# Kernel tuning notes

Measured on AMD Instinct MI355X. Metric: run time of the kernel, lower is better.

The kernel has to match this reference:

```python
import jax, jax.numpy as jnp
import numpy as np

N_HEADS, DK, DV, G = 12, 64, 64, 1
W_WIN, R_RAND = 3, 2
B, S, D = 2, 2048, 768


def _make_idx_tensor(seq_len, g, w, r, seed=0):
    # Mirrors SparseMultiHeadAttention.create_idx_tensor: each middle row is
    # [0] + r random key indices + w consecutive window key indices.
    rng = np.random.default_rng(seed)
    s2 = seq_len - 2 * g
    shift = max(g - (w - 1) // 2, 0)
    windows = np.arange(s2)[:, None] + np.arange(w)[None, :] + shift  # (s2, w)
    rand = np.empty((s2, r), np.int64)
    half = (w - 1) // 2
    for i in range(s2):
        pos = i + g
        cand = rng.choice(np.arange(1, seq_len), size=r + w + 2, replace=False)
        cand = cand[np.abs(cand - pos) > half][:r]
        rand[i] = cand
    idx = np.concatenate([np.zeros((s2, 1), np.int64), rand, windows], axis=1)
    return jnp.asarray(idx)  # (s2, 1+r+w)


def setup_inputs() -> dict:
    key = jax.random.key(0)
    ks = jax.random.split(key, 7)
    scale = 0.02  # keep projected logits in a sane range for softmax
    return {
        "Q": jax.random.normal(ks[0], (B, S, D), jnp.float32),
        "K": jax.random.normal(ks[1], (B, S, D), jnp.float32),
        "V": jax.random.normal(ks[2], (B, S, D), jnp.float32),
        "Wq": jax.random.normal(ks[3], (N_HEADS * DK, D), jnp.float32) * scale,
        "Wk": jax.random.normal(ks[4], (N_HEADS * DK, D), jnp.float32) * scale,
        "Wv": jax.random.normal(ks[5], (N_HEADS * DV, D), jnp.float32) * scale,
        "Wo": jax.random.normal(ks[6], (D, N_HEADS * DV), jnp.float32) * scale,
        "idx_tensor": _make_idx_tensor(S, G, W_WIN, R_RAND),
    }


def reference(Q, K, V, Wq, Wk, Wv, Wo, idx_tensor):
    b, s, d = Q.shape
    h, dk, dv, g = N_HEADS, DK, DV, G
    # projections (torch Linear: x @ W.T), split heads -> (b, h, s, d_head)
    q = (Q @ Wq.T).reshape(b, s, h, dk).transpose(0, 2, 1, 3)
    k = (K @ Wk.T).reshape(b, s, h, dk).transpose(0, 2, 1, 3)
    v = (V @ Wv.T).reshape(b, s, h, dv).transpose(0, 2, 1, 3)

    # global rows (first g, last g) attend densely over all keys
    gidx = jnp.concatenate([jnp.arange(g), jnp.arange(s - g, s)])
    global_attn = jnp.einsum('bhgd,bhtd->bhgt', q[:, :, gidx, :], k)  # (b,h,2g,s)

    # middle rows: gather [first, random..., window...] keys per row
    comb = k[:, :, idx_tensor, :]                    # (b, h, s2, 1+r+w, dk)
    scores = jnp.einsum('bhsd,bhskd->bhsk', q[:, :, g:s - g, :], comb)

    # scatter into a dense (s, s) score matrix (zeros elsewhere), as the source does
    result = jnp.zeros((b, h, s, s), q.dtype)
    result = result.at[:, :, gidx, :].set(global_attn)
    rows = jnp.arange(g, s - g)[:, None]             # (s2, 1)
    result = result.at[:, :, rows, idx_tensor].set(scores)
    result = result / jnp.sqrt(jnp.asarray(dk, q.dtype))

    attn = jax.nn.softmax(result, axis=-1)
    out = jnp.einsum('bhst,bhtd->bhsd', attn, v)     # (b, h, s, dv)
    out = out.transpose(0, 2, 1, 3).reshape(b, s, h * dv)
    return out @ Wo.T
```

## Files before the change

### kernel.cpp

```cpp
#include <hip/hip_runtime.h>
#include <hip/hip_bf16.h>

#define S_LEN   2048
#define D_MODEL 768
#define NH      12
#define HD      64
#define NI      6
#define S2      2046
#define BB      2
#define NCH     8
#define CHK     256

typedef unsigned short ushort_t;
typedef __attribute__((ext_vector_type(8))) short short8v;
typedef __attribute__((ext_vector_type(4))) float f32x4;

__device__ __forceinline__ unsigned short bf16_rne(float x) {
    union { float f; unsigned int u; } c; c.f = x;
    unsigned int u = c.u + 0x7fffu + ((c.u >> 16) & 1u);
    return (unsigned short)(u >> 16);
}
__device__ __forceinline__ float bf16_f(unsigned short h) {
    union { unsigned int u; float f; } c; c.u = ((unsigned int)h) << 16;
    return c.f;
}

__device__ __forceinline__ void gload16(const ushort_t* g, ushort_t* l) {
    __builtin_amdgcn_global_load_lds(
        (const __attribute__((address_space(1))) void*)g,
        (__attribute__((address_space(3))) void*)l, 16, 0, 0);
}

struct Cvt4 {
    const float* s0; const float* s1; const float* s2; const float* s3;
    ushort_t* d0; ushort_t* d1; ushort_t* d2; ushort_t* d3;
};

__global__ __launch_bounds__(256) void cvt_kernel(Cvt4 a, int n) {
    const float* s; ushort_t* d;
    switch (blockIdx.z) {
        case 0: s = a.s0; d = a.d0; break;
        case 1: s = a.s1; d = a.d1; break;
        case 2: s = a.s2; d = a.d2; break;
        default: s = a.s3; d = a.d3; break;
    }
    const int i = (blockIdx.x * 256 + threadIdx.x) * 8;
    float4 v0 = *(const float4*)&s[i];
    float4 v1 = *(const float4*)&s[i + 4];
    short8v o;
    o[0] = (short)bf16_rne(v0.x); o[1] = (short)bf16_rne(v0.y);
    o[2] = (short)bf16_rne(v0.z); o[3] = (short)bf16_rne(v0.w);
    o[4] = (short)bf16_rne(v1.x); o[5] = (short)bf16_rne(v1.y);
    o[6] = (short)bf16_rne(v1.z); o[7] = (short)bf16_rne(v1.w);
    *(short8v*)&d[i] = o;
}

struct GemmArgs { const ushort_t* A; const ushort_t* W; ushort_t* C; float* Cf; };

constexpr int GK = 768, GN = 768, GBK = 32, GNT = GK / GBK;

__global__ __launch_bounds__(256) void bf16_gemm_nt(GemmArgs g0, GemmArgs g1, GemmArgs g2) {
    GemmArgs g = (blockIdx.z == 0) ? g0 : ((blockIdx.z == 1) ? g1 : g2);

    __shared__ ushort_t As[3][4096];
    __shared__ ushort_t Bs[3][4096];

    const int tid  = threadIdx.x;
    const int lane = tid & 63;
    const int w    = tid >> 6;
    const int wm   = w & 1;
    const int wn   = w >> 1;
    const int bm   = blockIdx.y * 128;
    const int bn   = blockIdx.x * 128;
    const int fr   = lane & 15;
    const int blkr = lane >> 4;

    f32x4 acc[4][4];
    #pragma unroll
    for (int i = 0; i < 4; ++i)
        #pragma unroll
        for (int j = 0; j < 4; ++j)
            acc[i][j] = (f32x4){0.f, 0.f, 0.f, 0.f};

    const int row0 = tid >> 2;
    const int row1 = row0 + 64;
    const int blk0 = (tid & 3) ^ ((row0 >> 1) & 3);
    const int blk1 = (tid & 3) ^ ((row1 >> 1) & 3);
    const ushort_t* Ag0 = g.A + (size_t)(bm + row0) * GK + blk0 * 8;
    const ushort_t* Ag1 = g.A + (size_t)(bm + row1) * GK + blk1 * 8;
    const ushort_t* Bg0 = g.W + (size_t)(bn + row0) * GK + blk0 * 8;
    const ushort_t* Bg1 = g.W + (size_t)(bn + row1) * GK + blk1 * 8;
    const int l0 = w * 512;
    const int l1 = 2048 + w * 512;

    int aoff[4], boff[4];
    #pragma unroll
    for (int i = 0; i < 4; ++i) {
        const int ra = wm * 64 + i * 16 + fr;
        aoff[i] = (ra * 4 + (blkr ^ ((ra >> 1) & 3))) * 8;
        const int rb = wn * 64 + i * 16 + fr;
        boff[i] = (rb * 4 + (blkr ^ ((rb >> 1) & 3))) * 8;
    }

    gload16(Ag0, &As[0][l0]); gload16(Ag1, &As[0][l1]);
    gload16(Bg0, &Bs[0][l0]); gload16(Bg1, &Bs[0][l1]);
    gload16(Ag0 + GBK, &As[1][l0]); gload16(Ag1 + GBK, &As[1][l1]);
    gload16(Bg0 + GBK, &Bs[1][l0]); gload16(Bg1 + GBK, &Bs[1][l1]);

    for (int t = 0; t < GNT; ++t) {
        if (t < GNT - 1) asm volatile("s_waitcnt vmcnt(4)" ::: "memory");
        else             asm volatile("s_waitcnt vmcnt(0)" ::: "memory");
        __builtin_amdgcn_s_barrier();

        if (t + 2 < GNT) {
            const int ko = (t + 2) * GBK;
            const int nb = (t + 2) % 3;
            gload16(Ag0 + ko, &As[nb][l0]); gload16(Ag1 + ko, &As[nb][l1]);
            gload16(Bg0 + ko, &Bs[nb][l0]); gload16(Bg1 + ko, &Bs[nb][l1]);
        }

        const ushort_t* as = As[t % 3];
        const ushort_t* bs = Bs[t % 3];
        short8v a[4], b[4];
        #pragma unroll
        for (int i = 0; i < 4; ++i) a[i] = *(const short8v*)&as[aoff[i]];
        #pragma unroll
        for (int i = 0; i < 4; ++i) b[i] = *(const short8v*)&bs[boff[i]];
        #pragma unroll
        for (int i = 0; i < 4; ++i)
            #pragma unroll
            for (int j = 0; j < 4; ++j)
                acc[i][j] = __builtin_amdgcn_mfma_f32_16x16x32_bf16(a[i], b[j], acc[i][j], 0, 0, 0);
    }

    const int crow0 = bm + wm * 64 + ((lane >> 4) << 2);
    const int ccol0 = bn + wn * 64 + fr;
    if (g.Cf) {
        #pragma unroll
        for (int i = 0; i < 4; ++i)
            #pragma unroll
            for (int j = 0; j < 4; ++j)
                #pragma unroll
                for (int r = 0; r < 4; ++r)
                    g.Cf[(size_t)(crow0 + i * 16 + r) * GN + ccol0 + j * 16] = acc[i][j][r];
    } else {
        #pragma unroll
        for (int i = 0; i < 4; ++i)
            #pragma unroll
            for (int j = 0; j < 4; ++j)
                #pragma unroll
                for (int r = 0; r < 4; ++r)
                    g.C[(size_t)(crow0 + i * 16 + r) * GN + ccol0 + j * 16] = bf16_rne(acc[i][j][r]);
    }
}

__global__ __launch_bounds__(256) void vsum_kernel(const ushort_t* __restrict__ v,
                                                   float* __restrict__ vsum) {
    const int b = blockIdx.x;
    const int c = blockIdx.y * 256 + threadIdx.x;
    const int s0 = blockIdx.z * 64;
    float a = 0.f;
    for (int s = s0; s < s0 + 64; ++s)
        a += bf16_f(v[((size_t)(b * S_LEN + s)) * D_MODEL + c]);
    atomicAdd(&vsum[b * D_MODEL + c], a);
}

__global__ __launch_bounds__(768) void sparse_attn(
    const ushort_t* __restrict__ q, const ushort_t* __restrict__ k, const ushort_t* __restrict__ v,
    const float* __restrict__ vsum, const int* __restrict__ idx,
    ushort_t* __restrict__ ao) {
    const int i = blockIdx.x;
    const int b = blockIdx.y;
    const int pos = i + 1;
    const int c = threadIdx.x;

    int id[NI];
    #pragma unroll
    for (int j = 0; j < NI; ++j) id[j] = idx[i * NI + j];
    bool dup[NI];
    #pragma unroll
    for (int j = 0; j < NI; ++j) {
        bool d = false;
        #pragma unroll
        for (int j2 = 0; j2 < NI; ++j2)
            if (j2 < j) d = d || (id[j2] == id[j]);
        dup[j] = d;
    }

    const size_t rowbase = ((size_t)(b * S_LEN + pos)) * D_MODEL;
    const float qv = bf16_f(q[rowbase + c]);

    float kv[NI], vv[NI];
    #pragma unroll
    for (int j = 0; j < NI; ++j) {
        const size_t kb = ((size_t)(b * S_LEN + id[j])) * D_MODEL + c;
        kv[j] = bf16_f(k[kb]);
        vv[j] = bf16_f(v[kb]);
    }

    float p[NI];
    #pragma unroll
    for (int j = 0; j < NI; ++j) p[j] = qv * kv[j];

    #pragma unroll
    for (int off = 32; off; off >>= 1) {
        #pragma unroll
        for (int j = 0; j < NI; ++j) p[j] += __shfl_xor(p[j], off);
    }

    float acc = vsum[b * D_MODEL + c];
    float Z = 0.f;
    int u = 0;
    #pragma unroll
    for (int j = 0; j < NI; ++j) {
        if (dup[j]) continue;
        float e = expf(p[j] * 0.125f);
        Z += e;
        u += 1;
        acc += (e - 1.f) * vv[j];
    }
    Z += (float)(S_LEN - u);
    ao[rowbase + c] = bf16_rne(acc / Z);
}

__global__ __launch_bounds__(256) void global_attn_part(
    const ushort_t* __restrict__ q, const ushort_t* __restrict__ k, const ushort_t* __restrict__ v,
    float* __restrict__ part) {
    const int ch = blockIdx.x;
    const int rowsel = blockIdx.y;
    const int row = rowsel ? (S_LEN - 1) : 0;
    const int hb = blockIdx.z;
    const int h = hb % NH;
    const int b = hb / NH;
    const int tid = threadIdx.x;

    __shared__ float qs[HD];
    __shared__ float ps[CHK];
    __shared__ float red[8];
    __shared__ float pacc[256];

    if (tid < HD) qs[tid] = bf16_f(q[((size_t)(b * S_LEN + row)) * D_MODEL + h * HD + tid]);
    __syncthreads();

    const int t = ch * CHK + tid;
    const ushort_t* kp = &k[((size_t)(b * S_LEN + t)) * D_MODEL + h * HD];
    float s = 0.f;
    #pragma unroll
    for (int dd = 0; dd < 8; ++dd) {
        short8v kk = *(const short8v*)&kp[dd * 8];
        #pragma unroll
        for (int e = 0; e < 8; ++e)
            s += qs[dd * 8 + e] * bf16_f((unsigned short)kk[e]);
    }
    s *= 0.125f;

    float m = s;
    #pragma unroll
    for (int off = 32; off; off >>= 1) m = fmaxf(m, __shfl_xor(m, off));
    if ((tid & 63) == 0) red[tid >> 6] = m;
    __syncthreads();
    m = fmaxf(fmaxf(red[0], red[1]), fmaxf(red[2], red[3]));

    float e = expf(s - m);
    ps[tid] = e;
    float zp = e;
    #pragma unroll
    for (int off = 32; off; off >>= 1) zp += __shfl_xor(zp, off);
    if ((tid & 63) == 0) red[4 + (tid >> 6)] = zp;
    __syncthreads();
    const float E = red[4] + red[5] + red[6] + red[7];

    const int d0 = tid & 63;
    const int grp = tid >> 6;
    float acc = 0.f;
    for (int tt = grp; tt < CHK; tt += 4)
        acc += ps[tt] * bf16_f(v[((size_t)(b * S_LEN + ch * CHK + tt)) * D_MODEL + h * HD + d0]);
    pacc[tid] = acc;
    __syncthreads();
    if (tid < HD) {
        float o = pacc[tid] + pacc[64 + tid] + pacc[128 + tid] + pacc[192 + tid];
        float* pr = part + ((size_t)((hb * 2 + rowsel) * NCH + ch)) * (HD + 2);
        pr[2 + tid] = o;
        if (tid == 0) { pr[0] = m; pr[1] = E; }
    }
}

__global__ __launch_bounds__(64) void global_attn_fin(
    const float* __restrict__ part, ushort_t* __restrict__ ao) {
    const int rb = blockIdx.x;
    const int rowsel = rb & 1;
    const int hb = rb >> 1;
    const int h = hb % NH;
    const int b = hb / NH;
    const int row = rowsel ? (S_LEN - 1) : 0;
    const int d = threadIdx.x;

    const float* pr = part + (size_t)rb * NCH * (HD + 2);
    float M = -1e30f;
    #pragma unroll
    for (int c = 0; c < NCH; ++c) M = fmaxf(M, pr[c * (HD + 2)]);
    float Z = 0.f, acc = 0.f;
    #pragma unroll
    for (int c = 0; c < NCH; ++c) {
        float wgt = expf(pr[c * (HD + 2)] - M);
        Z   += pr[c * (HD + 2) + 1] * wgt;
        acc += pr[c * (HD + 2) + 2 + d] * wgt;
    }
    ao[((size_t)(b * S_LEN + row)) * D_MODEL + h * HD + d] = bf16_rne(acc / Z);
}

extern "C" void kernel_launch(void* const* d_in, const int* in_sizes, int n_in,
                              void* d_out, int out_size, void* d_ws, size_t ws_size,
                              hipStream_t stream) {
    const float* Q  = (const float*)d_in[0];
    const float* K  = (const float*)d_in[1];
    const float* V  = (const float*)d_in[2];
    const float* Wq = (const float*)d_in[3];
    const float* Wk = (const float*)d_in[4];
    const float* Wv = (const float*)d_in[5];
    const float* Wo = (const float*)d_in[6];
    const int*  idx = (const int*)d_in[7];
    float* out = (float*)d_out;

    const size_t SZ  = (size_t)BB * S_LEN * D_MODEL;
    const size_t WSZ = (size_t)D_MODEL * D_MODEL;

    ushort_t* Qc  = (ushort_t*)d_ws;
    ushort_t* Kc  = Qc  + SZ;
    ushort_t* Vc  = Kc  + SZ;
    ushort_t* Wqc = Vc  + SZ;
    ushort_t* Wkc = Wqc + WSZ;
    ushort_t* Wvc = Wkc + WSZ;
    ushort_t* Woc = Wvc + WSZ;
    ushort_t* qb  = Woc + WSZ;
    ushort_t* kb  = qb  + SZ;
    ushort_t* vb  = kb  + SZ;
    ushort_t* ao  = vb  + SZ;
    float* vs   = (float*)(ao + SZ);
    float* part = vs + BB * D_MODEL;

    {
        Cvt4 a{Q, K, V, Q, Qc, Kc, Vc, Qc};
        cvt_kernel<<<dim3((unsigned)(SZ / 2048), 1, 3), 256, 0, stream>>>(a, (int)SZ);
        Cvt4 b{Wq, Wk, Wv, Wo, Wqc, Wkc, Wvc, Woc};
        cvt_kernel<<<dim3((unsigned)(WSZ / 2048), 1, 4), 256, 0, stream>>>(b, (int)WSZ);
    }

    hipMemsetAsync(vs, 0, BB * D_MODEL * sizeof(float), stream);

    {
        GemmArgs g0{Qc, Wqc, qb, nullptr}, g1{Kc, Wkc, kb, nullptr}, g2{Vc, Wvc, vb, nullptr};
        bf16_gemm_nt<<<dim3(D_MODEL / 128, BB * S_LEN / 128, 3), 256, 0, stream>>>(g0, g1, g2);
    }
    vsum_kernel<<<dim3(BB, D_MODEL / 256, 32), 256, 0, stream>>>(vb, vs);
    sparse_attn<<<dim3(S2, BB), 768, 0, stream>>>(qb, kb, vb, vs, idx, ao);
    global_attn_part<<<dim3(NCH, 2, NH * BB), 256, 0, stream>>>(qb, kb, vb, part);
    global_attn_fin<<<dim3(2 * NH * BB), 64, 0, stream>>>(part, ao);
    {
        GemmArgs g{ao, Woc, nullptr, out};
        bf16_gemm_nt<<<dim3(D_MODEL / 128, BB * S_LEN / 128, 1), 256, 0, stream>>>(g, g, g);
    }
}
```

Baseline: 214.5 us.

## Merge conversions, fuse V column-sum into GEMM epilogue, batch sparse rows

```diff
diff --git a/kernel.cpp b/kernel.cpp
--- a/kernel.cpp
+++ b/kernel.cpp
@@ -31,20 +31,36 @@
         (__attribute__((address_space(3))) void*)l, 16, 0, 0);
 }
 
-struct Cvt4 {
-    const float* s0; const float* s1; const float* s2; const float* s3;
-    ushort_t* d0; ushort_t* d1; ushort_t* d2; ushort_t* d3;
+struct CvtAll {
+    const float* Q; const float* K; const float* V;
+    const float* Wq; const float* Wk; const float* Wv; const float* Wo;
+    ushort_t* Qc; ushort_t* Kc; ushort_t* Vc;
+    ushort_t* Wqc; ushort_t* Wkc; ushort_t* Wvc; ushort_t* Woc;
+    float* vs;
 };
 
-__global__ __launch_bounds__(256) void cvt_kernel(Cvt4 a, int n) {
-    const float* s; ushort_t* d;
-    switch (blockIdx.z) {
-        case 0: s = a.s0; d = a.d0; break;
-        case 1: s = a.s1; d = a.d1; break;
-        case 2: s = a.s2; d = a.d2; break;
-        default: s = a.s3; d = a.d3; break;
-    }
-    const int i = (blockIdx.x * 256 + threadIdx.x) * 8;
+__global__ __launch_bounds__(256) void cvt_all(CvtAll a) {
+    const int z = blockIdx.z;
+    const int tid = threadIdx.x;
+    if (z == 4) {
+        if (blockIdx.x == 0)
+            for (int i = tid; i < BB * D_MODEL; i += 256) a.vs[i] = 0.f;
+        return;
+    }
+    const float* s; ushort_t* d; long i;
+    if (z < 3) {
+        s = (z == 0) ? a.Q : (z == 1) ? a.K : a.V;
+        d = (z == 0) ? a.Qc : (z == 1) ? a.Kc : a.Vc;
+        i = ((long)blockIdx.x * 256 + tid) * 8;
+    } else {
+        const long WSZ = (long)D_MODEL * D_MODEL;
+        long f = ((long)blockIdx.x * 256 + tid) * 8;
+        if (f >= 4 * WSZ) return;
+        const int which = (int)(f / WSZ);
+        i = f % WSZ;
+        s = (which == 0) ? a.Wq : (which == 1) ? a.Wk : (which == 2) ? a.Wv : a.Wo;
+        d = (which == 0) ? a.Wqc : (which == 1) ? a.Wkc : (which == 2) ? a.Wvc : a.Woc;
+    }
     float4 v0 = *(const float4*)&s[i];
     float4 v1 = *(const float4*)&s[i + 4];
     short8v o;
@@ -55,7 +71,7 @@
     *(short8v*)&d[i] = o;
 }
 
-struct GemmArgs { const ushort_t* A; const ushort_t* W; ushort_t* C; float* Cf; };
+struct GemmArgs { const ushort_t* A; const ushort_t* W; ushort_t* C; float* Cf; float* vs; };
 
 constexpr int GK = 768, GN = 768, GBK = 32, GNT = GK / GBK;
 
@@ -151,76 +167,90 @@
                 #pragma unroll
                 for (int r = 0; r < 4; ++r)
                     g.C[(size_t)(crow0 + i * 16 + r) * GN + ccol0 + j * 16] = bf16_rne(acc[i][j][r]);
-    }
-}
-
-__global__ __launch_bounds__(256) void vsum_kernel(const ushort_t* __restrict__ v,
-                                                   float* __restrict__ vsum) {
-    const int b = blockIdx.x;
-    const int c = blockIdx.y * 256 + threadIdx.x;
-    const int s0 = blockIdx.z * 64;
-    float a = 0.f;
-    for (int s = s0; s < s0 + 64; ++s)
-        a += bf16_f(v[((size_t)(b * S_LEN + s)) * D_MODEL + c]);
-    atomicAdd(&vsum[b * D_MODEL + c], a);
+        if (g.vs) {
+            const int bsel = (bm >= S_LEN) ? 1 : 0;
+            #pragma unroll
+            for (int j = 0; j < 4; ++j) {
+                float part = 0.f;
+                #pragma unroll
+                for (int i = 0; i < 4; ++i)
+                    #pragma unroll
+                    for (int r = 0; r < 4; ++r)
+                        part += bf16_f(bf16_rne(acc[i][j][r]));
+                atomicAdd(&g.vs[bsel * D_MODEL + ccol0 + j * 16], part);
+            }
+        }
+    }
 }
 
 __global__ __launch_bounds__(768) void sparse_attn(
     const ushort_t* __restrict__ q, const ushort_t* __restrict__ k, const ushort_t* __restrict__ v,
     const float* __restrict__ vsum, const int* __restrict__ idx,
     ushort_t* __restrict__ ao) {
-    const int i = blockIdx.x;
+    const int i0 = blockIdx.x * 2;
     const int b = blockIdx.y;
-    const int pos = i + 1;
     const int c = threadIdx.x;
 
-    int id[NI];
-    #pragma unroll
-    for (int j = 0; j < NI; ++j) id[j] = idx[i * NI + j];
-    bool dup[NI];
-    #pragma unroll
-    for (int j = 0; j < NI; ++j) {
-        bool d = false;
-        #pragma unroll
-        for (int j2 = 0; j2 < NI; ++j2)
-            if (j2 < j) d = d || (id[j2] == id[j]);
-        dup[j] = d;
-    }
-
-    const size_t rowbase = ((size_t)(b * S_LEN + pos)) * D_MODEL;
-    const float qv = bf16_f(q[rowbase + c]);
-
-    float kv[NI], vv[NI];
-    #pragma unroll
-    for (int j = 0; j < NI; ++j) {
-        const size_t kb = ((size_t)(b * S_LEN + id[j])) * D_MODEL + c;
-        kv[j] = bf16_f(k[kb]);
-        vv[j] = bf16_f(v[kb]);
-    }
-
-    float p[NI];
-    #pragma unroll
-    for (int j = 0; j < NI; ++j) p[j] = qv * kv[j];
+    int id[2][NI];
+    #pragma unroll
+    for (int r = 0; r < 2; ++r)
+        #pragma unroll
+        for (int j = 0; j < NI; ++j) id[r][j] = idx[(i0 + r) * NI + j];
+    bool dup[2][NI];
+    #pragma unroll
+    for (int r = 0; r < 2; ++r)
+        #pragma unroll
+        for (int j = 0; j < NI; ++j) {
+            bool d = false;
+            #pragma unroll
+            for (int j2 = 0; j2 < NI; ++j2)
+                if (j2 < j) d = d || (id[r][j2] == id[r][j]);
+            dup[r][j] = d;
+        }
+
+    const size_t rb0 = ((size_t)(b * S_LEN + i0 + 1)) * D_MODEL + c;
+    const float qv0 = bf16_f(q[rb0]);
+    const float qv1 = bf16_f(q[rb0 + D_MODEL]);
+
+    float kv[2][NI], vv[2][NI];
+    #pragma unroll
+    for (int r = 0; r < 2; ++r)
+        #pragma unroll
+        for (int j = 0; j < NI; ++j) {
+            const size_t kb = ((size_t)(b * S_LEN + id[r][j])) * D_MODEL + c;
+            kv[r][j] = bf16_f(k[kb]);
+            vv[r][j] = bf16_f(v[kb]);
+        }
+
+    float p[2][NI];
+    #pragma unroll
+    for (int j = 0; j < NI; ++j) { p[0][j] = qv0 * kv[0][j]; p[1][j] = qv1 * kv[1][j]; }
 
     #pragma unroll
     for (int off = 32; off; off >>= 1) {
         #pragma unroll
-        for (int j = 0; j < NI; ++j) p[j] += __shfl_xor(p[j], off);
-    }
-
-    float acc = vsum[b * D_MODEL + c];
-    float Z = 0.f;
-    int u = 0;
-    #pragma unroll
-    for (int j = 0; j < NI; ++j) {
-        if (dup[j]) continue;
-        float e = expf(p[j] * 0.125f);
-        Z += e;
-        u += 1;
-        acc += (e - 1.f) * vv[j];
-    }
-    Z += (float)(S_LEN - u);
-    ao[rowbase + c] = bf16_rne(acc / Z);
+        for (int r = 0; r < 2; ++r)
+            #pragma unroll
+            for (int j = 0; j < NI; ++j) p[r][j] += __shfl_xor(p[r][j], off);
+    }
+
+    const float vsc = vsum[b * D_MODEL + c];
+    #pragma unroll
+    for (int r = 0; r < 2; ++r) {
+        float acc = vsc;
+        float Z = 0.f;
+        int u = 0;
+        #pragma unroll
+        for (int j = 0; j < NI; ++j) {
+            if (dup[r][j]) continue;
+            float e = expf(p[r][j] * 0.125f);
+            Z += e;
+            u += 1;
+            acc += (e - 1.f) * vv[r][j];
+        }
+        Z += (float)(S_LEN - u);
+        ao[rb0 + (size_t)r * D_MODEL] = bf16_rne(acc / Z);
+    }
 }
 
 __global__ __launch_bounds__(256) void global_attn_part(
@@ -237,7 +267,7 @@
     __shared__ float qs[HD];
     __shared__ float ps[CHK];
     __shared__ float red[8];
-    __shared__ float pacc[256];
+    __shared__ float redv[32][72];
 
     if (tid < HD) qs[tid] = bf16_f(q[((size_t)(b * S_LEN + row)) * D_MODEL + h * HD + tid]);
     __syncthreads();
@@ -270,15 +300,23 @@
     __syncthreads();
     const float E = red[4] + red[5] + red[6] + red[7];
 
-    const int d0 = tid & 63;
-    const int grp = tid >> 6;
-    float acc = 0.f;
-    for (int tt = grp; tt < CHK; tt += 4)
-        acc += ps[tt] * bf16_f(v[((size_t)(b * S_LEN + ch * CHK + tt)) * D_MODEL + h * HD + d0]);
-    pacc[tid] = acc;
+    const int g8 = tid >> 3;
+    const int d8 = (tid & 7) * 8;
+    float a8[8] = {};
+    for (int tt = g8; tt < CHK; tt += 32) {
+        const float wgt = ps[tt];
+        short8v v8 = *(const short8v*)&v[((size_t)(b * S_LEN + ch * CHK + tt)) * D_MODEL + h * HD + d8];
+        #pragma unroll
+        for (int e2 = 0; e2 < 8; ++e2)
+            a8[e2] += wgt * bf16_f((unsigned short)v8[e2]);
+    }
+    #pragma unroll
+    for (int e2 = 0; e2 < 8; ++e2) redv[g8][d8 + e2] = a8[e2];
     __syncthreads();
     if (tid < HD) {
-        float o = pacc[tid] + pacc[64 + tid] + pacc[128 + tid] + pacc[192 + tid];
+        float o = 0.f;
+        #pragma unroll
+        for (int gg = 0; gg < 32; ++gg) o += redv[gg][tid];
         float* pr = part + ((size_t)((hb * 2 + rowsel) * NCH + ch)) * (HD + 2);
         pr[2 + tid] = o;
         if (tid == 0) { pr[0] = m; pr[1] = E; }
@@ -340,24 +378,20 @@
     float* part = vs + BB * D_MODEL;
 
     {
-        Cvt4 a{Q, K, V, Q, Qc, Kc, Vc, Qc};
-        cvt_kernel<<<dim3((unsigned)(SZ / 2048), 1, 3), 256, 0, stream>>>(a, (int)SZ);
-        Cvt4 b{Wq, Wk, Wv, Wo, Wqc, Wkc, Wvc, Woc};
-        cvt_kernel<<<dim3((unsigned)(WSZ / 2048), 1, 4), 256, 0, stream>>>(b, (int)WSZ);
-    }
-
-    hipMemsetAsync(vs, 0, BB * D_MODEL * sizeof(float), stream);
-
+        CvtAll a{Q, K, V, Wq, Wk, Wv, Wo, Qc, Kc, Vc, Wqc, Wkc, Wvc, Woc, vs};
+        cvt_all<<<dim3((unsigned)(SZ / 2048), 1, 5), 256, 0, stream>>>(a);
+    }
     {
-        GemmArgs g0{Qc, Wqc, qb, nullptr}, g1{Kc, Wkc, kb, nullptr}, g2{Vc, Wvc, vb, nullptr};
+        GemmArgs g0{Qc, Wqc, qb, nullptr, nullptr};
+        GemmArgs g1{Kc, Wkc, kb, nullptr, nullptr};
+        GemmArgs g2{Vc, Wvc, vb, nullptr, vs};
         bf16_gemm_nt<<<dim3(D_MODEL / 128, BB * S_LEN / 128, 3), 256, 0, stream>>>(g0, g1, g2);
     }
-    vsum_kernel<<<dim3(BB, D_MODEL / 256, 32), 256, 0, stream>>>(vb, vs);
-    sparse_attn<<<dim3(S2, BB), 768, 0, stream>>>(qb, kb, vb, vs, idx, ao);
+    sparse_attn<<<dim3(S2 / 2, BB), 768, 0, stream>>>(qb, kb, vb, vs, idx, ao);
     global_attn_part<<<dim3(NCH, 2, NH * BB), 256, 0, stream>>>(qb, kb, vb, part);
     global_attn_fin<<<dim3(2 * NH * BB), 64, 0, stream>>>(part, ao);
     {
-        GemmArgs g{ao, Woc, nullptr, out};
+        GemmArgs g{ao, Woc, nullptr, out, nullptr};
         bf16_gemm_nt<<<dim3(D_MODEL / 128, BB * S_LEN / 128, 1), 256, 0, stream>>>(g, g, g);
     }
 }
```

Result: faster. 198.2 us (-7.6%).
